# Optimization experiments

Measured on AMD Instinct MI355X. Metric: run time of the kernel, lower is better.

## Reference

```python
import jax, jax.numpy as jnp
import numpy as np
import math

B, S, DM = 32, 512, 1024   # batch (= groups*channels), seq_len, d_model
H, D, C = 16, 64, 8        # n_heads, d_kv, n_channels
NB, MD = 32, 128           # relative_attention_num_buckets, max_distance


def setup_inputs() -> dict:
    key = jax.random.key(0)
    ks = jax.random.split(key, 7)
    return {
        "hidden_states": jax.random.normal(ks[0], (B, S, DM), jnp.float32),
        "Wq": jax.random.normal(ks[1], (DM, H * D), jnp.float32) * 0.02,
        "Wk": jax.random.normal(ks[2], (DM, H * D), jnp.float32) * 0.02,
        "Wv": jax.random.normal(ks[3], (DM, H * D), jnp.float32) * 0.02,
        "Wo": jax.random.normal(ks[4], (H * D, DM), jnp.float32) * 0.02,
        "rel_emb": jax.random.normal(ks[5], (NB, H), jnp.float32) * 0.02,
        "beta": jax.random.normal(ks[6], (1, 1, H, 1, 1), jnp.float32) * 0.01,
    }


def _rel_bucket(relative_position, num_buckets=NB, max_distance=MD):
    # bidirectional (encoder) bucketing, faithful to T5
    nb = num_buckets // 2
    buckets = (relative_position > 0).astype(jnp.int32) * nb
    rp = jnp.abs(relative_position)
    max_exact = nb // 2
    is_small = rp < max_exact
    rp_safe = jnp.maximum(rp, 1).astype(jnp.float32)
    large = max_exact + (
        jnp.log(rp_safe / max_exact) / math.log(max_distance / max_exact) * (nb - max_exact)
    ).astype(jnp.int32)
    large = jnp.minimum(large, nb - 1)
    return buckets + jnp.where(is_small, rp, large)


def reference(hidden_states, Wq, Wk, Wv, Wo, rel_emb, beta):
    G = B // C  # groups

    def proj(W):
        # (B,S,DM) -> (B,S,H,D) -> (B,H,S,D) -> (G,C,H,S,D)
        x = (hidden_states @ W).reshape(B, S, H, D).transpose(0, 2, 1, 3)
        return x.reshape(G, C, H, S, D)

    q, k, v = proj(Wq), proj(Wk), proj(Wv)

    # relative position bias: (1,1,H,S,S)
    rel_pos = jnp.arange(S)[None, :] - jnp.arange(S)[:, None]
    bias = rel_emb[_rel_bucket(rel_pos)].transpose(2, 0, 1)[None, None]

    # local (dot-product) attention, T5-style: no 1/sqrt(d) scaling
    scores = jnp.einsum('gchsd,gchtd->gchst', q, k) + bias
    attn_w = jax.nn.softmax(scores, axis=-1)
    a_dot = jnp.einsum('gchst,gchtd->gchsd', attn_w, v)

    # compressive memory: ELU+1 feature map, summed over channels
    sk = jax.nn.elu(k) + 1.0
    M = jnp.einsum('gchsd,gchse->ghde', sk, v)   # (G,H,D,D)
    z = sk.sum(axis=3).sum(axis=1)               # (G,H,D)
    sq = jax.nn.elu(q) + 1.0
    num = jnp.einsum('gchsd,ghde->gchse', sq, M)
    den = jnp.einsum('gchsd,ghd->gchs', sq, z)[..., None] + 1e-6
    a_mem = num / den

    gate = jax.nn.sigmoid(beta)  # (1,1,H,1,1)
    out = gate * a_mem + (1.0 - gate) * a_dot

    # (G,C,H,S,D) -> (B,H,S,D) -> (B,S,H*D)
    out = out.reshape(B, H, S, D).transpose(0, 2, 1, 3).reshape(B, S, H * D)
    return out @ Wo
```

## Files before the change

### kernel.cpp

```cpp
#include <hip/hip_runtime.h>
#include <stdint.h>

typedef unsigned short u16;
typedef u16 u16x8 __attribute__((ext_vector_type(8)));
typedef u16 u16x4 __attribute__((ext_vector_type(4)));
typedef __bf16 bf16x8 __attribute__((ext_vector_type(8)));
typedef float f32x4 __attribute__((ext_vector_type(4)));

#define DEV static __device__ __forceinline__

DEV u16 f2bf(float f) {
  union { float f; uint32_t u; } v; v.f = f;
  uint32_t r = v.u + 0x7FFFu + ((v.u >> 16) & 1u);
  return (u16)(r >> 16);
}
DEV float bf2f(u16 s) {
  union { uint32_t u; float f; } v; v.u = ((uint32_t)s) << 16;
  return v.f;
}
DEV float elu1(float x) { return x > 0.f ? x + 1.f : __expf(x); }
DEV u16x8 ld8u(const u16* p) { return *reinterpret_cast<const u16x8*>(p); }

DEV f32x4 mfma16(u16x8 a, u16x8 b, f32x4 c) {
  return __builtin_amdgcn_mfma_f32_16x16x32_bf16(
      __builtin_bit_cast(bf16x8, a), __builtin_bit_cast(bf16x8, b), c, 0, 0, 0);
}
DEV void async16(void* lds, const void* g) {
  __builtin_amdgcn_global_load_lds(
      (__attribute__((address_space(1))) void*)g,
      (__attribute__((address_space(3))) void*)lds, 16, 0, 0);
}


__global__ __launch_bounds__(256) void k_cvt(const float* __restrict__ in, u16* __restrict__ out) {
  int i = blockIdx.x * 256 + threadIdx.x;
  const float4* p = reinterpret_cast<const float4*>(in) + (size_t)i * 2;
  float4 a = p[0], b = p[1];
  u16x8 o;
  o[0] = f2bf(a.x); o[1] = f2bf(a.y); o[2] = f2bf(a.z); o[3] = f2bf(a.w);
  o[4] = f2bf(b.x); o[5] = f2bf(b.y); o[6] = f2bf(b.z); o[7] = f2bf(b.w);
  reinterpret_cast<u16x8*>(out)[i] = o;
}

__global__ __launch_bounds__(1024) void k_tr(const float* __restrict__ Wq, const float* __restrict__ Wk,
                                             const float* __restrict__ Wv, const float* __restrict__ Wo,
                                             u16* __restrict__ wt, u16* __restrict__ wot) {
  __shared__ float tb[32][33];
  int mat = blockIdx.x >> 10;
  int tile = blockIdx.x & 1023;
  int n0 = (tile >> 5) * 32;
  int k0 = (tile & 31) * 32;
  const float* W = (mat == 0) ? Wq : (mat == 1) ? Wk : (mat == 2) ? Wv : Wo;
  int tx = threadIdx.x & 31, ty = threadIdx.x >> 5;
  tb[ty][tx] = W[(size_t)(k0 + ty) * 1024 + n0 + tx];
  __syncthreads();
  u16 v = f2bf(tb[tx][ty]);
  if (mat < 3) wt[(size_t)(mat * 1024 + n0 + ty) * 1024 + k0 + tx] = v;
  else         wot[(size_t)(n0 + ty) * 1024 + k0 + tx] = v;
}

__global__ void k_bias(const float* __restrict__ rel, float* __restrict__ bias) {
  int off = blockIdx.x * 256 + threadIdx.x;
  if (off >= 1023) return;
  int rp = off - 511;
  int bck = rp > 0 ? 16 : 0;
  int arp = rp < 0 ? -rp : rp;
  int idx;
  if (arp < 8) idx = arp;
  else {
    float l = logf((float)arp * 0.125f) / logf(16.0f) * 8.0f;
    int lg = 8 + (int)l;
    idx = lg < 15 ? lg : 15;
  }
  bck += idx;
  for (int h = 0; h < 16; ++h) bias[h * 1023 + off] = rel[bck * 16 + h];
}


#define BARR __builtin_amdgcn_s_barrier()
#define LG0  asm volatile("s_waitcnt lgkmcnt(0)" ::: "memory")
#define VMC(N) asm volatile("s_waitcnt vmcnt(" #N ")" ::: "memory")

template <int EPI, int NBN, int CPX>
__global__ __launch_bounds__(512, 2) void k_g256(const u16* __restrict__ A, const u16* __restrict__ Bt,
                                                 u16* __restrict__ oq, u16* __restrict__ ok2,
                                                 u16* __restrict__ ovt, float* __restrict__ of) {
  __shared__ __align__(16) u16 lsA[2][256 * 64];
  __shared__ __align__(16) u16 lsB[2][256 * 64];
  const int t = threadIdx.x;
  const int lane = t & 63, w = t >> 6;
  const int wm = w >> 2, wn = w & 3;
  const int lr = lane & 15, lg = lane >> 4;
  const int rI = t >> 3, uu = t & 7;

  const int bid = blockIdx.x;
  const int wg = (bid & 7) * CPX + (bid >> 3);
  const int m0 = (wg / NBN) * 256;
  const int n0 = (wg % NBN) * 256;

  auto stA = [&](int kt, int slot, int half) {
    const int k0 = kt * 64;
#pragma unroll
    for (int i = 0; i < 2; ++i) {
      int row = half * 64 + i * 128 + rI;
      async16(&lsA[slot][row * 64 + uu * 8],
              A + (size_t)(m0 + row) * 1024 + k0 + ((uu ^ (row & 7)) << 3));
    }
  };
  auto stB = [&](int kt, int slot, int half) {
    const int k0 = kt * 64;
#pragma unroll
    for (int i = 0; i < 2; ++i) {
      int row = half * 32 + i * 128 + (rI >> 5) * 64 + (rI & 31);
      async16(&lsB[slot][row * 64 + uu * 8],
              Bt + (size_t)(n0 + row) * 1024 + k0 + ((uu ^ (row & 7)) << 3));
    }
  };

  f32x4 acc[8][4];
#pragma unroll
  for (int i = 0; i < 8; ++i)
#pragma unroll
    for (int j = 0; j < 4; ++j) acc[i][j] = (f32x4){0.f, 0.f, 0.f, 0.f};

#define RDA(la, grp, af)                                                      \
  _Pragma("unroll") for (int mi = 0; mi < 4; ++mi) {                          \
    const int r_ = wm * 128 + (grp) * 64 + mi * 16 + lr;                      \
    _Pragma("unroll") for (int kk = 0; kk < 2; ++kk)                          \
        af[mi][kk] = ld8u((la) + r_ * 64 + (((kk * 4 + lg) ^ (r_ & 7)) << 3));\
  }
#define RDB(lb, grp, bf)                                                      \
  _Pragma("unroll") for (int ni = 0; ni < 2; ++ni) {                          \
    const int r_ = wn * 64 + ((grp) * 2 + ni) * 16 + lr;                      \
    _Pragma("unroll") for (int kk = 0; kk < 2; ++kk)                          \
        bf[ni][kk] = ld8u((lb) + r_ * 64 + (((kk * 4 + lg) ^ (r_ & 7)) << 3));\
  }
#define MM(af, bf, MB, NB_)                                                   \
  __builtin_amdgcn_s_setprio(1);                                              \
  _Pragma("unroll") for (int mi = 0; mi < 4; ++mi)                            \
  _Pragma("unroll") for (int ni = 0; ni < 2; ++ni)                            \
  _Pragma("unroll") for (int kk = 0; kk < 2; ++kk)                            \
      acc[(MB) + mi][(NB_) + ni] =                                            \
          mfma16(af[mi][kk], bf[ni][kk], acc[(MB) + mi][(NB_) + ni]);         \
  __builtin_amdgcn_s_setprio(0);

  stA(0, 0, 0); stB(0, 0, 0); stB(0, 0, 1); stA(0, 0, 1); stA(1, 1, 0);
  VMC(6);
  BARR;

  for (int T = 0; T < 14; ++T) {
    const int slot = T & 1, os = slot ^ 1;
    const u16* la = &lsA[slot][0];
    const u16* lb = &lsB[slot][0];
    u16x8 a0[4][2], a1[4][2], b0[2][2], b1[2][2];
    RDB(lb, 0, b0); RDA(la, 0, a0);
    stB(T + 1, os, 0);
    BARR; LG0;
    MM(a0, b0, 0, 0);
    VMC(6); BARR;
    RDB(lb, 1, b1);
    stB(T + 1, os, 1);
    BARR; LG0;
    MM(a0, b1, 0, 2);
    VMC(6); BARR;
    RDA(la, 1, a1);
    stA(T + 1, os, 1);
    BARR; LG0;
    MM(a1, b0, 4, 0);
    BARR;
    stA(T + 2, slot, 0);
    BARR; LG0;
    MM(a1, b1, 4, 2);
    VMC(6); BARR;
  }
  {
    const u16* la = &lsA[0][0];
    const u16* lb = &lsB[0][0];
    u16x8 a0[4][2], a1[4][2], b0[2][2], b1[2][2];
    RDB(lb, 0, b0); RDA(la, 0, a0);
    stB(15, 1, 0);
    BARR; LG0;
    MM(a0, b0, 0, 0);
    VMC(6); BARR;
    RDB(lb, 1, b1);
    stB(15, 1, 1);
    BARR; LG0;
    MM(a0, b1, 0, 2);
    VMC(6); BARR;
    RDA(la, 1, a1);
    stA(15, 1, 1);
    BARR; LG0;
    MM(a1, b0, 4, 0);
    BARR;
    BARR; LG0;
    MM(a1, b1, 4, 2);
    VMC(4); BARR;
  }
  {
    const u16* la = &lsA[1][0];
    const u16* lb = &lsB[1][0];
    u16x8 a0[4][2], a1[4][2], b0[2][2], b1[2][2];
    RDB(lb, 0, b0); RDA(la, 0, a0);
    BARR; LG0;
    MM(a0, b0, 0, 0);
    VMC(2); BARR;
    RDB(lb, 1, b1);
    BARR; LG0;
    MM(a0, b1, 0, 2);
    VMC(0); BARR;
    RDA(la, 1, a1);
    BARR; LG0;
    MM(a1, b0, 4, 0);
    MM(a1, b1, 4, 2);
  }

  if (EPI == 0) {
    const int which = n0 >> 10;
    const int nb = (n0 & 1023) + wn * 64;
#pragma unroll
    for (int mi = 0; mi < 8; ++mi)
#pragma unroll
      for (int r = 0; r < 4; ++r) {
        int m = m0 + wm * 128 + mi * 16 + lg * 4 + r;
        int b = m >> 9, s = m & 511;
#pragma unroll
        for (int ni = 0; ni < 4; ++ni) {
          int nc = nb + ni * 16 + lr;
          int h = nc >> 6, d = nc & 63;
          int bh = b * 16 + h;
          u16 v = f2bf(acc[mi][ni][r]);
          if (which == 0)      oq[(size_t)(bh * 512 + s) * 64 + d] = v;
          else if (which == 1) ok2[(size_t)(bh * 512 + s) * 64 + d] = v;
          else                 ovt[(size_t)(bh * 64 + d) * 512 + s] = v;
        }
      }
  } else {
#pragma unroll
    for (int mi = 0; mi < 8; ++mi)
#pragma unroll
      for (int r = 0; r < 4; ++r) {
        int m = m0 + wm * 128 + mi * 16 + lg * 4 + r;
#pragma unroll
        for (int ni = 0; ni < 4; ++ni) {
          int n = n0 + wn * 64 + ni * 16 + lr;
          of[(size_t)m * 1024 + n] = acc[mi][ni][r];
        }
      }
  }
}


__global__ __launch_bounds__(256) void k_mem(const u16* __restrict__ K, const u16* __restrict__ Vt,
                                             float* __restrict__ Mp, float* __restrict__ zp) {
  __shared__ __align__(16) float sk[128 * 64];
  __shared__ __align__(16) float vv[128 * 64];
  const int bid = blockIdx.x;
  const int g = bid >> 7, h = (bid >> 3) & 15, c = bid & 7;
  const int bh = (g * 8 + c) * 16 + h;
  const u16* kp = K + (size_t)bh * 512 * 64;
  const u16* vp = Vt + (size_t)bh * 64 * 512;
  const int t = threadIdx.x;
  const int d = t & 63, eg = t >> 6;
  float acc[16];
#pragma unroll
  for (int j = 0; j < 16; ++j) acc[j] = 0.f;
  float zacc = 0.f;

  for (int s0 = 0; s0 < 512; s0 += 128) {
    __syncthreads();
    for (int j = 0; j < 32; ++j) {
      int idx = j * 256 + t;
      int ss = idx >> 6, dd = idx & 63;
      sk[idx] = elu1(bf2f(kp[(size_t)(s0 + ss) * 64 + dd]));
      int ee = idx >> 7, s2 = idx & 127;
      vv[s2 * 64 + ee] = bf2f(vp[(size_t)ee * 512 + s0 + s2]);
    }
    __syncthreads();
    for (int ss = 0; ss < 128; ++ss) {
      float a = sk[ss * 64 + d];
      if (eg == 0) zacc += a;
      const f32x4* vr = reinterpret_cast<const f32x4*>(&vv[ss * 64 + eg * 16]);
#pragma unroll
      for (int j4 = 0; j4 < 4; ++j4) {
        f32x4 vq = vr[j4];
        acc[j4 * 4 + 0] += a * vq[0];
        acc[j4 * 4 + 1] += a * vq[1];
        acc[j4 * 4 + 2] += a * vq[2];
        acc[j4 * 4 + 3] += a * vq[3];
      }
    }
  }
  float* mp = Mp + (size_t)bid * 4096 + d * 64 + eg * 16;
#pragma unroll
  for (int j = 0; j < 16; ++j) mp[j] = acc[j];
  if (eg == 0) zp[(size_t)bid * 64 + d] = zacc;
}

__global__ __launch_bounds__(256) void k_red(const float* __restrict__ Mp, const float* __restrict__ zp,
                                             u16* __restrict__ Mt, float* __restrict__ zv) {
  const int gh = blockIdx.x;
  const int t = threadIdx.x;
#pragma unroll
  for (int j = 0; j < 16; ++j) {
    int idx = j * 256 + t;
    int d = idx >> 6, e = idx & 63;
    float s = 0.f;
#pragma unroll
    for (int c = 0; c < 8; ++c) s += Mp[(size_t)(gh * 8 + c) * 4096 + idx];
    Mt[(size_t)gh * 4096 + e * 64 + d] = f2bf(s);
  }
  if (t < 64) {
    float s = 0.f;
#pragma unroll
    for (int c = 0; c < 8; ++c) s += zp[(size_t)(gh * 8 + c) * 64 + t];
    zv[gh * 64 + t] = s;
  }
}


__global__ __launch_bounds__(256, 4) void k_attn(const u16* __restrict__ Q, const u16* __restrict__ K,
                                                 const u16* __restrict__ Vt, const u16* __restrict__ Mt,
                                                 const float* __restrict__ zv, const float* __restrict__ bias,
                                                 const float* __restrict__ beta, u16* __restrict__ blend) {
  __shared__ __align__(16) u16 lK[64 * 64];
  __shared__ __align__(16) u16 lV[64 * 64];
  __shared__ __align__(16) u16 ps[4][32 * 64];
  __shared__ float lbias[1023];
  __shared__ float zs[64];
  __shared__ float rsl[4][32];
  __shared__ float dnl[4][32];

  const int bid = blockIdx.x;
  const int bh = bid >> 2, qg = bid & 3;
  const int b = bh >> 4, h = bh & 15, g = b >> 3;
  const int gh = g * 16 + h;
  const int t = threadIdx.x, lane = t & 63, w = t >> 6;
  const int lr = lane & 15, lg = lane >> 4;
  const int q0w = qg * 128 + w * 32;
  const u16* qp = Q + (size_t)bh * 512 * 64;
  const u16* kp = K + (size_t)bh * 512 * 64;
  const u16* vp = Vt + (size_t)bh * 64 * 512;
  const u16* mp = Mt + (size_t)gh * 4096;
  const float gate = 1.f / (1.f + __expf(-beta[h]));
  u16* psw = &ps[w][0];

  for (int i = t; i < 1023; i += 256) lbias[i] = bias[h * 1023 + i];
  if (t < 64) zs[t] = zv[gh * 64 + t];

  u16x8 qf[2][2];
#pragma unroll
  for (int qs = 0; qs < 2; ++qs)
#pragma unroll
    for (int dc = 0; dc < 2; ++dc)
      qf[qs][dc] = ld8u(qp + (size_t)(q0w + qs * 16 + lr) * 64 + dc * 32 + lg * 8);

#pragma unroll
  for (int i = 0; i < 2; ++i) {
    int c = w * 128 + i * 64 + lane;
    int kr = c >> 3, u = c & 7;
    async16(lK + c * 8, kp + (size_t)kr * 64 + ((u ^ (kr & 7)) << 3));
    async16(lV + c * 8, vp + (size_t)kr * 512 + ((u ^ (kr & 7)) << 3));
  }
  __syncthreads();

#pragma unroll
  for (int qs = 0; qs < 2; ++qs) {
    float sum = 0.f;
#pragma unroll
    for (int dc = 0; dc < 2; ++dc)
#pragma unroll
      for (int j = 0; j < 8; ++j)
        sum += elu1(bf2f(qf[qs][dc][j])) * zs[dc * 32 + lg * 8 + j];
    sum += __shfl_xor(sum, 16, 64);
    sum += __shfl_xor(sum, 32, 64);
    if (lane < 16) dnl[w][qs * 16 + lane] = sum + 1e-6f;
  }

  f32x4 acc[2][4];
#pragma unroll
  for (int qs = 0; qs < 2; ++qs)
#pragma unroll
    for (int es = 0; es < 4; ++es) acc[qs][es] = (f32x4){0.f, 0.f, 0.f, 0.f};
  float rs[2] = {0.f, 0.f};

  for (int kt = 0; kt < 8; ++kt) {
#pragma unroll
    for (int ks = 0; ks < 4; ++ks) {
      const int kr = ks * 16 + lr;
      u16x8 kf0 = ld8u(lK + kr * 64 + (((0 * 4 + lg) ^ (kr & 7)) << 3));
      u16x8 kf1 = ld8u(lK + kr * 64 + (((1 * 4 + lg) ^ (kr & 7)) << 3));
#pragma unroll
      for (int qs = 0; qs < 2; ++qs) {
        f32x4 s = mfma16(kf0, qf[qs][0], (f32x4){0.f, 0.f, 0.f, 0.f});
        s = mfma16(kf1, qf[qs][1], s);
        const int bbase = kt * 64 + ks * 16 + lg * 4 - (q0w + qs * 16 + lr) + 511;
        u16x4 pk;
        float lsum = 0.f;
#pragma unroll
        for (int r = 0; r < 4; ++r) {
          float p = __expf(s[r] + lbias[bbase + r]);
          lsum += p;
          pk[r] = f2bf(p);
        }
        rs[qs] += lsum;
        const int row = qs * 16 + lr;
        const int addr = row * 64 + (((ks * 2 + (lg >> 1)) ^ (row & 7)) << 3) + (lg & 1) * 4;
        *reinterpret_cast<u16x4*>(psw + addr) = pk;
      }
    }
#pragma unroll
    for (int kc = 0; kc < 2; ++kc) {
      u16x8 pf[2];
#pragma unroll
      for (int qs = 0; qs < 2; ++qs) {
        const int row = qs * 16 + lr;
        pf[qs] = ld8u(psw + row * 64 + (((kc * 4 + lg) ^ (row & 7)) << 3));
      }
#pragma unroll
      for (int es = 0; es < 4; ++es) {
        const int er = es * 16 + lr;
        u16x8 vf = ld8u(lV + er * 64 + (((kc * 4 + lg) ^ (er & 7)) << 3));
#pragma unroll
        for (int qs = 0; qs < 2; ++qs) acc[qs][es] = mfma16(pf[qs], vf, acc[qs][es]);
      }
    }
    __syncthreads();
    if (kt + 1 < 8) {
#pragma unroll
      for (int i = 0; i < 2; ++i) {
        int c = w * 128 + i * 64 + lane;
        int kr = c >> 3, u = c & 7;
        async16(lK + c * 8, kp + (size_t)((kt + 1) * 64 + kr) * 64 + ((u ^ (kr & 7)) << 3));
        async16(lV + c * 8, vp + (size_t)kr * 512 + (kt + 1) * 64 + ((u ^ (kr & 7)) << 3));
      }
    }
    __syncthreads();
  }

#pragma unroll
  for (int qs = 0; qs < 2; ++qs) {
    float v = rs[qs];
    v += __shfl_xor(v, 16, 64);
    v += __shfl_xor(v, 32, 64);
    if (lane < 16) rsl[w][qs * 16 + lane] = 1.f / v;
  }

  u16x8 sqf[2][2];
#pragma unroll
  for (int qs = 0; qs < 2; ++qs)
#pragma unroll
    for (int dc = 0; dc < 2; ++dc)
#pragma unroll
      for (int j = 0; j < 8; ++j) sqf[qs][dc][j] = f2bf(elu1(bf2f(qf[qs][dc][j])));
  f32x4 am[2][4];
#pragma unroll
  for (int qs = 0; qs < 2; ++qs)
#pragma unroll
    for (int es = 0; es < 4; ++es) am[qs][es] = (f32x4){0.f, 0.f, 0.f, 0.f};
#pragma unroll
  for (int es = 0; es < 4; ++es)
#pragma unroll
    for (int dc = 0; dc < 2; ++dc) {
      u16x8 mf = ld8u(mp + (es * 16 + lr) * 64 + dc * 32 + lg * 8);
#pragma unroll
      for (int qs = 0; qs < 2; ++qs) am[qs][es] = mfma16(sqf[qs][dc], mf, am[qs][es]);
    }

#pragma unroll
  for (int qs = 0; qs < 2; ++qs)
#pragma unroll
    for (int r = 0; r < 4; ++r) {
      const int rowl = qs * 16 + lg * 4 + r;
      const float rinv = rsl[w][rowl];
      const float den = dnl[w][rowl];
      const int q = q0w + rowl;
#pragma unroll
      for (int es = 0; es < 4; ++es) {
        float o = gate * (am[qs][es][r] / den) + (1.f - gate) * acc[qs][es][r] * rinv;
        blend[(size_t)(b * 512 + q) * 1024 + h * 64 + es * 16 + lr] = f2bf(o);
      }
    }
}


extern "C" void kernel_launch(void* const* d_in, const int* in_sizes, int n_in,
                              void* d_out, int out_size, void* d_ws, size_t ws_size,
                              hipStream_t stream) {
  (void)in_sizes; (void)n_in; (void)out_size; (void)ws_size;
  const float* hs   = (const float*)d_in[0];
  const float* Wq   = (const float*)d_in[1];
  const float* Wk   = (const float*)d_in[2];
  const float* Wv   = (const float*)d_in[3];
  const float* Wo   = (const float*)d_in[4];
  const float* rel  = (const float*)d_in[5];
  const float* beta = (const float*)d_in[6];
  float* out = (float*)d_out;

  char* ws = (char*)d_ws;
  size_t off = 0;
  auto alloc = [&](size_t bytes) -> char* {
    char* p = ws + off;
    off += (bytes + 255) & ~(size_t)255;
    return p;
  };
  u16* hsb    = (u16*)alloc(16384ull * 1024 * 2);
  u16* wt     = (u16*)alloc(3072ull * 1024 * 2);
  u16* wot    = (u16*)alloc(1024ull * 1024 * 2);
  u16* q      = (u16*)alloc(16384ull * 1024 * 2);
  u16* k      = (u16*)alloc(16384ull * 1024 * 2);
  u16* vt     = (u16*)alloc(16384ull * 1024 * 2);
  float* Mp   = (float*)alloc(512ull * 4096 * 4);
  float* zp   = (float*)alloc(512ull * 64 * 4);
  u16* Mt     = (u16*)alloc(64ull * 4096 * 2);
  float* zv   = (float*)alloc(64ull * 64 * 4);
  float* bias = (float*)alloc(16ull * 1023 * 4);
  u16* blend  = hsb;

  k_cvt<<<8192, 256, 0, stream>>>(hs, hsb);
  k_tr<<<4096, 1024, 0, stream>>>(Wq, Wk, Wv, Wo, wt, wot);
  k_bias<<<4, 256, 0, stream>>>(rel, bias);
  k_g256<0, 12, 96><<<768, 512, 0, stream>>>(hsb, wt, q, k, vt, nullptr);
  k_mem<<<512, 256, 0, stream>>>(k, vt, Mp, zp);
  k_red<<<64, 256, 0, stream>>>(Mp, zp, Mt, zv);
  k_attn<<<2048, 256, 0, stream>>>(q, k, vt, Mt, zv, bias, beta, blend);
  k_g256<1, 4, 32><<<256, 512, 0, stream>>>(blend, wot, nullptr, nullptr, nullptr, out);
}
```

Measured before the change: 407.7 us.

## Restructure GEMM pipeline to stage whole k-tiles two ahead in one batch

The GEMM main loop previously interleaved partial A/B half-tile async loads between each MFMA sub-block, with unrolled prologue and epilogue iterations. It now issues all loads for tile T+2 in a single batch after the third MFMA group and waits once per iteration, folding the tail iterations into one 16-step loop. This simplifies the schedule and gives the loads a longer, unbroken window to complete. In exchange, loads are no longer spread across the iteration, which may cause bursts of memory traffic and more exposed latency per tile.

```diff
diff --git a/kernel.cpp b/kernel.cpp
--- a/kernel.cpp
+++ b/kernel.cpp
@@ -116,6 +116,9 @@
               Bt + (size_t)(n0 + row) * 1024 + k0 + ((uu ^ (row & 7)) << 3));
     }
   };
+  auto stageAll = [&](int kt, int slot) {
+    stA(kt, slot, 0); stA(kt, slot, 1); stB(kt, slot, 0); stB(kt, slot, 1);
+  };
 
   f32x4 acc[8][4];
 #pragma unroll
@@ -144,74 +147,34 @@
           mfma16(af[mi][kk], bf[ni][kk], acc[(MB) + mi][(NB_) + ni]);         \
   __builtin_amdgcn_s_setprio(0);
 
-  stA(0, 0, 0); stB(0, 0, 0); stB(0, 0, 1); stA(0, 0, 1); stA(1, 1, 0);
-  VMC(6);
+  stageAll(0, 0);
+  stageAll(1, 1);
+  VMC(8);
   BARR;
 
-  for (int T = 0; T < 14; ++T) {
-    const int slot = T & 1, os = slot ^ 1;
+  for (int T = 0; T < 16; ++T) {
+    const int slot = T & 1;
     const u16* la = &lsA[slot][0];
     const u16* lb = &lsB[slot][0];
     u16x8 a0[4][2], a1[4][2], b0[2][2], b1[2][2];
     RDB(lb, 0, b0); RDA(la, 0, a0);
-    stB(T + 1, os, 0);
     BARR; LG0;
     MM(a0, b0, 0, 0);
-    VMC(6); BARR;
+    BARR;
     RDB(lb, 1, b1);
-    stB(T + 1, os, 1);
     BARR; LG0;
     MM(a0, b1, 0, 2);
-    VMC(6); BARR;
+    BARR;
     RDA(la, 1, a1);
-    stA(T + 1, os, 1);
     BARR; LG0;
     MM(a1, b0, 4, 0);
     BARR;
-    stA(T + 2, slot, 0);
-    BARR; LG0;
+    if (T < 14) stageAll(T + 2, slot);
+    BARR;
     MM(a1, b1, 4, 2);
-    VMC(6); BARR;
-  }
-  {
-    const u16* la = &lsA[0][0];
-    const u16* lb = &lsB[0][0];
-    u16x8 a0[4][2], a1[4][2], b0[2][2], b1[2][2];
-    RDB(lb, 0, b0); RDA(la, 0, a0);
-    stB(15, 1, 0);
-    BARR; LG0;
-    MM(a0, b0, 0, 0);
-    VMC(6); BARR;
-    RDB(lb, 1, b1);
-    stB(15, 1, 1);
-    BARR; LG0;
-    MM(a0, b1, 0, 2);
-    VMC(6); BARR;
-    RDA(la, 1, a1);
-    stA(15, 1, 1);
-    BARR; LG0;
-    MM(a1, b0, 4, 0);
+    if (T < 14)      { VMC(8); }
+    else if (T == 14){ VMC(0); }
     BARR;
-    BARR; LG0;
-    MM(a1, b1, 4, 2);
-    VMC(4); BARR;
-  }
-  {
-    const u16* la = &lsA[1][0];
-    const u16* lb = &lsB[1][0];
-    u16x8 a0[4][2], a1[4][2], b0[2][2], b1[2][2];
-    RDB(lb, 0, b0); RDA(la, 0, a0);
-    BARR; LG0;
-    MM(a0, b0, 0, 0);
-    VMC(2); BARR;
-    RDB(lb, 1, b1);
-    BARR; LG0;
-    MM(a0, b1, 0, 2);
-    VMC(0); BARR;
-    RDA(la, 1, a1);
-    BARR; LG0;
-    MM(a1, b0, 4, 0);
-    MM(a1, b1, 4, 2);
   }
 
   if (EPI == 0) {
```

Measured after the change: 421.2 us. 1.03x slower.
